# Performance work log

Hardware: AMD Instinct MI355X
Metric: run time of the kernel (lower is better)

Reference implementation:

```python
import jax, jax.numpy as jnp
import numpy as np

C_IN = 34   # C*V = 2*17 channels after reshape
C_MID = 16
C_OUT = 3
N_LAYERS = 3
BN_EPS = 1e-5
NEG_SLOPE = 0.01


def setup_inputs() -> dict:
    key = jax.random.key(0)
    ks = jax.random.split(key, 16)
    B, C, T, V = 512, 2, 2048, 17
    s = 1.0 / np.sqrt(C_IN)
    inp = {
        "x": jax.random.normal(ks[0], (B, C, T, V), dtype=jnp.float32),
        # stacked per-layer 1x1-conv (linear) weights for Q/K/V of 3 attention layers
        "wq": jax.random.normal(ks[1], (N_LAYERS, C_IN, C_IN), dtype=jnp.float32) * s,
        "bq": jax.random.normal(ks[2], (N_LAYERS, C_IN), dtype=jnp.float32) * 0.02,
        "wk": jax.random.normal(ks[3], (N_LAYERS, C_IN, C_IN), dtype=jnp.float32) * s,
        "bk": jax.random.normal(ks[4], (N_LAYERS, C_IN), dtype=jnp.float32) * 0.02,
        "wv": jax.random.normal(ks[5], (N_LAYERS, C_IN, C_IN), dtype=jnp.float32) * s,
        "bv": jax.random.normal(ks[6], (N_LAYERS, C_IN), dtype=jnp.float32) * 0.02,
        # head: conv1 -> BN -> LeakyReLU -> conv2
        "w1": jax.random.normal(ks[7], (C_MID, C_IN), dtype=jnp.float32) * s,
        "b1": jax.random.normal(ks[8], (C_MID,), dtype=jnp.float32) * 0.02,
        "gamma": jnp.ones((C_MID,), dtype=jnp.float32),
        "beta": jnp.zeros((C_MID,), dtype=jnp.float32),
        "mean": jax.random.normal(ks[9], (C_MID,), dtype=jnp.float32) * 0.1,
        "var": jax.random.uniform(ks[10], (C_MID,), dtype=jnp.float32, minval=0.5, maxval=1.5),
        "w2": jax.random.normal(ks[11], (C_OUT, C_MID), dtype=jnp.float32) * (1.0 / np.sqrt(C_MID)),
        "b2": jax.random.normal(ks[12], (C_OUT,), dtype=jnp.float32) * 0.02,
    }
    return inp


def _conv1x1(w, b, h):
    # 1x1 Conv1d == linear over channel dim: (O,C) x (B,C,T) -> (B,O,T)
    return jnp.einsum('oc,bct->bot', w, h) + b[:, None]


def reference(x, wq, bq, wk, bk, wv, bv, w1, b1, gamma, beta, mean, var, w2, b2):
    B, C, T, V = x.shape
    h = x.transpose(0, 1, 3, 2).reshape(B, C * V, T)  # (B, 34, T)
    scale = 1.0 / (T ** 0.5)  # K.size(-1) ** 0.5 in the original
    for i in range(N_LAYERS):
        Q = _conv1x1(wq[i], bq[i], h)
        K = _conv1x1(wk[i], bk[i], h)
        Vv = _conv1x1(wv[i], bv[i], h)
        scores = jnp.einsum('bct,bdt->bcd', Q, K) * scale  # (B, 34, 34) channel attention
        attn = jax.nn.softmax(scores, axis=-1)
        h = jnp.einsum('bcd,bdt->bct', attn, Vv)
    y = _conv1x1(w1, b1, h)                               # (B, 16, T)
    inv = gamma / jnp.sqrt(var + BN_EPS)                  # inference-mode BatchNorm1d
    y = (y - mean[:, None]) * inv[:, None] + beta[:, None]
    y = jnp.where(y > 0, y, NEG_SLOPE * y)                # LeakyReLU
    return _conv1x1(w2, b2, y)                            # (B, 3, T)
```

## Files before the change

kernel.cpp:

```cpp
#include <hip/hip_runtime.h>

#define CV   34
#define TTOT 2048
#define NB   512
#define XB   69632
#define XC   34816

#define GS_STRIDE 1192
#define RB_OFF    (512 * 1192)
#define RB_STRIDE 576

typedef __attribute__((ext_vector_type(8))) short v8s;
typedef __attribute__((ext_vector_type(4))) float v4f;

__device__ __forceinline__ unsigned short f2bf(float f) {
    unsigned int u = __float_as_uint(f);
    u = u + 0x7FFFu + ((u >> 16) & 1u);
    return (unsigned short)(u >> 16);
}
__device__ __forceinline__ float bf2f(unsigned short s) {
    return __uint_as_float(((unsigned int)s) << 16);
}

__device__ __forceinline__ unsigned int cvtpk_bf16(float a, float b) {
    unsigned int r;
    asm("v_cvt_pk_bf16_f32 %0, %1, %2" : "=v"(r) : "v"(a), "v"(b));
    return r;
}

__device__ __forceinline__ void split8(const float (&f)[8], v8s* hi, v8s* lo) {
    union { unsigned int u[4]; v8s s; } H, L;
#pragma unroll
    for (int p = 0; p < 4; ++p) {
        float a = f[2 * p], b = f[2 * p + 1];
        unsigned int h = cvtpk_bf16(a, b);
        float ra = a - __uint_as_float(h << 16);
        float rb = b - __uint_as_float(h & 0xFFFF0000u);
        L.u[p] = cvtpk_bf16(ra, rb);
        H.u[p] = h;
    }
    *hi = H.s;
    *lo = L.s;
}

__device__ __forceinline__ void stage_chunk(const float* __restrict__ xb, int t0,
                                            float* rawbuf, int w, int lane) {
#pragma unroll
    for (int i = 0; i < 5; ++i) {
        int idx = i * 4 + w;
        if (idx < 17) {
            int fl = idx * 256 + lane * 4;
            int co = (fl >= 2176) ? 1 : 0;
            const float* g = xb + t0 * 17 + fl + co * 32640;
            __builtin_amdgcn_global_load_lds(
                (const __attribute__((address_space(1))) void*)g,
                (__attribute__((address_space(3))) void*)(rawbuf + idx * 256),
                16, 0, 0);
        }
    }
}

struct SmemGramB {
    float Gpart[4][34][36];
    float spart[4][36];
};

__global__ __launch_bounds__(256, 4) void k_gram(const float* __restrict__ x,
                                                 float* __restrict__ ws) {
    __shared__ __align__(16) union {
        float raw[2][4352];
        SmemGramB b;
    } sm;

    const int b    = blockIdx.x >> 2;
    const int seg  = blockIdx.x & 3;
    const int tid  = threadIdx.x;
    const int l    = tid & 63;
    const int w    = tid >> 6;
    const int row16 = l & 15;
    const int quad  = l >> 4;
    const float* xb = x + (size_t)b * XB;
    const int t0 = seg * 512;

    int offc[3];
#pragma unroll
    for (int r = 0; r < 3; ++r) {
        int c = r * 16 + row16;
        if (c > 33) c = 33;
        offc[r] = (c >= 17) ? (2159 + c) : c;
    }
    const int koff = w * 32 + quad * 8;

    v4f accG[3][3];
    v4f accS[3];
    v4f vz = {0.f, 0.f, 0.f, 0.f};
#pragma unroll
    for (int r = 0; r < 3; ++r) {
        accS[r] = vz;
#pragma unroll
        for (int c = 0; c < 3; ++c) accG[r][c] = vz;
    }
    v8s ones;
#pragma unroll
    for (int i = 0; i < 8; ++i) ones[i] = (short)0x3F80;

    stage_chunk(xb, t0, sm.raw[0], w, l);
    __syncthreads();

    for (int ch = 0; ch < 4; ++ch) {
        const int cur = ch & 1;
        if (ch < 3) stage_chunk(xb, t0 + (ch + 1) * 128, sm.raw[cur ^ 1], w, l);

        const float* rb = sm.raw[cur] + koff * 17;
        v8s fh[3], fl4[3];
#pragma unroll
        for (int r = 0; r < 3; ++r) {
            const float* p = rb + offc[r];
            float f[8];
#pragma unroll
            for (int e = 0; e < 8; ++e) f[e] = p[e * 17];
            split8(f, &fh[r], &fl4[r]);
        }
#pragma unroll
        for (int r = 0; r < 3; ++r) {
#pragma unroll
            for (int c = 0; c < 3; ++c) {
                accG[r][c] = __builtin_amdgcn_mfma_f32_16x16x32_bf16(fh[r],  fh[c],  accG[r][c], 0, 0, 0);
                accG[r][c] = __builtin_amdgcn_mfma_f32_16x16x32_bf16(fh[r],  fl4[c], accG[r][c], 0, 0, 0);
                accG[r][c] = __builtin_amdgcn_mfma_f32_16x16x32_bf16(fl4[r], fh[c],  accG[r][c], 0, 0, 0);
            }
            accS[r] = __builtin_amdgcn_mfma_f32_16x16x32_bf16(fh[r],  ones, accS[r], 0, 0, 0);
            accS[r] = __builtin_amdgcn_mfma_f32_16x16x32_bf16(fl4[r], ones, accS[r], 0, 0, 0);
        }
        __syncthreads();
    }

#pragma unroll
    for (int r = 0; r < 3; ++r) {
#pragma unroll
        for (int c = 0; c < 3; ++c) {
#pragma unroll
            for (int i = 0; i < 4; ++i) {
                int m = r * 16 + quad * 4 + i;
                int n = c * 16 + row16;
                if (m < 34 && n < 34) sm.b.Gpart[w][m][n] = accG[r][c][i];
            }
        }
        if (row16 == 0) {
#pragma unroll
            for (int i = 0; i < 4; ++i) {
                int m = r * 16 + quad * 4 + i;
                if (m < 34) sm.b.spart[w][m] = accS[r][i];
            }
        }
    }
    __syncthreads();
    float* gout = ws + (size_t)b * GS_STRIDE;
    for (int idx = tid; idx < 1156; idx += 256) {
        int m = idx / 34, n = idx - m * 34;
        atomicAdd(&gout[idx], sm.b.Gpart[0][m][n] + sm.b.Gpart[1][m][n] +
                              sm.b.Gpart[2][m][n] + sm.b.Gpart[3][m][n]);
    }
    if (tid < 34)
        atomicAdd(&gout[1156 + tid], sm.b.spart[0][tid] + sm.b.spart[1][tid] +
                                     sm.b.spart[2][tid] + sm.b.spart[3][tid]);
}

#define RST 44
#define RSZ (36 * RST)
#define R_G0 0
#define R_At (1 * RSZ)
#define R_Aq (2 * RSZ)
#define R_Ak (3 * RSZ)
#define R_Av (4 * RSZ)
#define R_S1 (5 * RSZ)
#define R_Sc (6 * RSZ)
#define R_Wx (7 * RSZ)
#define SMF  (8 * RSZ)

__device__ __forceinline__ void ldfrag8(const float* p, v8s* hi, v8s* lo) {
    float f[8];
    *(float4*)&f[0] = *(const float4*)p;
    *(float4*)&f[4] = *(const float4*)(p + 4);
    split8(f, hi, lo);
}

__device__ __forceinline__ void ldfrag4(const float* p, int quad, v8s* hi, v8s* lo) {
    union { unsigned int u[4]; v8s s; } H, L;
#pragma unroll
    for (int i = 0; i < 4; ++i) { H.u[i] = 0; L.u[i] = 0; }
    if (quad == 0) {
        float4 f = *(const float4*)p;
        unsigned int h0 = cvtpk_bf16(f.x, f.y);
        unsigned int h1 = cvtpk_bf16(f.z, f.w);
        float r0 = f.x - __uint_as_float(h0 << 16);
        float r1 = f.y - __uint_as_float(h0 & 0xFFFF0000u);
        float r2 = f.z - __uint_as_float(h1 << 16);
        float r3 = f.w - __uint_as_float(h1 & 0xFFFF0000u);
        H.u[0] = h0; H.u[1] = h1;
        L.u[0] = cvtpk_bf16(r0, r1);
        L.u[1] = cvtpk_bf16(r2, r3);
    }
    *hi = H.s;
    *lo = L.s;
}

__device__ __forceinline__ void mfma_mm(float* __restrict__ SMD, int Lo, int Ro,
                                        int Do, int l, bool transD) {
    const int lc = l & 15, quad = l >> 4;
    v8s Bh0[3], Bl0[3], Bh1[3], Bl1[3];
#pragma unroll
    for (int tn = 0; tn < 3; ++tn) {
        int r = tn * 16 + lc; r = r < 36 ? r : 35;
        const float* p = SMD + Ro + r * RST;
        ldfrag8(p + quad * 8, &Bh0[tn], &Bl0[tn]);
        ldfrag4(p + 32, quad, &Bh1[tn], &Bl1[tn]);
    }
#pragma unroll
    for (int tm = 0; tm < 3; ++tm) {
        int r = tm * 16 + lc; r = r < 36 ? r : 35;
        const float* p = SMD + Lo + r * RST;
        v8s Ah0, Al0, Ah1, Al1;
        ldfrag8(p + quad * 8, &Ah0, &Al0);
        ldfrag4(p + 32, quad, &Ah1, &Al1);
#pragma unroll
        for (int tn = 0; tn < 3; ++tn) {
            v4f acc = {0.f, 0.f, 0.f, 0.f};
            acc = __builtin_amdgcn_mfma_f32_16x16x32_bf16(Ah0, Bh0[tn], acc, 0, 0, 0);
            acc = __builtin_amdgcn_mfma_f32_16x16x32_bf16(Ah0, Bl0[tn], acc, 0, 0, 0);
            acc = __builtin_amdgcn_mfma_f32_16x16x32_bf16(Al0, Bh0[tn], acc, 0, 0, 0);
            acc = __builtin_amdgcn_mfma_f32_16x16x32_bf16(Ah1, Bh1[tn], acc, 0, 0, 0);
            acc = __builtin_amdgcn_mfma_f32_16x16x32_bf16(Ah1, Bl1[tn], acc, 0, 0, 0);
            acc = __builtin_amdgcn_mfma_f32_16x16x32_bf16(Al1, Bh1[tn], acc, 0, 0, 0);
            if (!transD) {
                int gcol = tn * 16 + lc;
                if (gcol < 36) {
#pragma unroll
                    for (int i = 0; i < 4; ++i) {
                        int grow = tm * 16 + quad * 4 + i;
                        if (grow < 36) SMD[Do + grow * RST + gcol] = acc[i];
                    }
                }
            } else {
                int trow = tn * 16 + lc;
                int tcol = tm * 16 + quad * 4;
                if (trow < 36 && tcol < 36)
                    *(v4f*)&SMD[Do + trow * RST + tcol] = acc;
            }
        }
    }
}

__global__ __launch_bounds__(64) void k_chain(
    const float* __restrict__ wq, const float* __restrict__ bq,
    const float* __restrict__ wk, const float* __restrict__ bk,
    const float* __restrict__ wv, const float* __restrict__ bv,
    const float* __restrict__ w1, const float* __restrict__ b1,
    const float* __restrict__ gamma, const float* __restrict__ beta,
    const float* __restrict__ mean, const float* __restrict__ var,
    float* __restrict__ ws) {
    __shared__ __align__(16) float SMD[SMF];
    const int l = threadIdx.x;
    const int b = blockIdx.x;
    const float* gsb = ws + (size_t)b * GS_STRIDE;

    {
        const float4 z = make_float4(0.f, 0.f, 0.f, 0.f);
        for (int i = l * 4; i < SMF; i += 256) *(float4*)(SMD + i) = z;
    }
    __syncthreads();
    for (int idx = l; idx < 1156; idx += 64) {
        int m = idx / 34, n = idx - m * 34;
        SMD[R_G0 + m * RST + n] = gsb[idx];
        SMD[R_Aq + m * RST + n] = wq[idx];
        SMD[R_Ak + m * RST + n] = wk[idx];
        SMD[R_Av + n * RST + m] = wv[idx];
    }
    if (l < 34) {
        float s = gsb[1156 + l];
        SMD[R_G0 + 34 * RST + l] = s;
        SMD[R_G0 + l * RST + 34] = s;
        SMD[R_Aq + l * RST + 34] = bq[l];
        SMD[R_Ak + l * RST + 34] = bk[l];
        SMD[R_Av + 34 * RST + l] = bv[l];
    }
    if (l == 0) SMD[R_G0 + 34 * RST + 34] = 2048.0f;
    __syncthreads();

    for (int lyr = 0; lyr < 3; ++lyr) {
        if (lyr > 0) {
            const float* wql = wq + lyr * 1156;
            const float* wkl = wk + lyr * 1156;
            const float* wvl = wv + lyr * 1156;
            for (int idx = l; idx < 1156; idx += 64) {
                int m = idx / 34, n = idx - m * 34;
                SMD[R_S1 + m * RST + n] = wql[idx];
                SMD[R_Sc + m * RST + n] = wkl[idx];
                SMD[R_Wx + m * RST + n] = wvl[idx];
            }
            __syncthreads();
            mfma_mm(SMD, R_S1, R_At, R_Aq, l, false);
            mfma_mm(SMD, R_Sc, R_At, R_Ak, l, false);
            mfma_mm(SMD, R_Wx, R_At, R_Av, l, true);
            __syncthreads();
            if (l < 34) {
                SMD[R_Aq + l * RST + 34] += bq[lyr * 34 + l];
                SMD[R_Ak + l * RST + 34] += bk[lyr * 34 + l];
                SMD[R_Av + 34 * RST + l] += bv[lyr * 34 + l];
            }
            __syncthreads();
        }
        mfma_mm(SMD, R_Aq, R_G0, R_S1, l, false);
        __syncthreads();
        mfma_mm(SMD, R_S1, R_Ak, R_Sc, l, false);
        __syncthreads();
        if (l < 34) {
            float f[36];
#pragma unroll
            for (int e0 = 0; e0 < 36; e0 += 4)
                *(float4*)&f[e0] = *(const float4*)&SMD[R_Sc + l * RST + e0];
            const float scale = 0.022097086912079608f;
            float mx = -1e30f;
#pragma unroll
            for (int d = 0; d < 34; ++d) { f[d] *= scale; mx = fmaxf(mx, f[d]); }
            float sum = 0.f;
#pragma unroll
            for (int d = 0; d < 34; ++d) { float e = __expf(f[d] - mx); f[d] = e; sum += e; }
            float rs = 1.0f / sum;
#pragma unroll
            for (int d = 0; d < 34; ++d) f[d] *= rs;
            f[34] = 0.f; f[35] = 0.f;
#pragma unroll
            for (int e0 = 0; e0 < 36; e0 += 4)
                *(float4*)&SMD[R_Sc + l * RST + e0] = *(const float4*)&f[e0];
        } else if (l >= 36 && l < 54) {
            int u = l - 36;
            int row = 34 + u / 9, c4 = (u - (u / 9) * 9) * 4;
            *(float4*)&SMD[R_Sc + row * RST + c4] = make_float4(0.f, 0.f, 0.f, 0.f);
        }
        __syncthreads();
        mfma_mm(SMD, R_Av, R_Sc, R_At, l, false);
        __syncthreads();
    }

    for (int idx = l; idx < 544; idx += 64) {
        int m = idx / 34, n = idx - m * 34;
        SMD[R_Sc + m * RST + n] = w1[idx];
    }
    __syncthreads();
    mfma_mm(SMD, R_Sc, R_At, R_S1, l, false);
    __syncthreads();
    float* wb = ws + RB_OFF + (size_t)b * RB_STRIDE;
    if (l < 16) {
        float iv = gamma[l] * rsqrtf(var[l] + 1e-5f);
        float cyraw = SMD[R_S1 + l * RST + 34] + b1[l];
        wb[512 + l] = (cyraw - mean[l]) * iv + beta[l];
        wb[528 + l] = SMD[R_S1 + l * RST + 32] * iv;
        wb[544 + l] = SMD[R_S1 + l * RST + 33] * iv;
    }
    unsigned short* wp = (unsigned short*)wb;
    for (int i = l; i < 512; i += 64) {
        int o = i >> 5, c = i & 31;
        float iv = gamma[o] * rsqrtf(var[o] + 1e-5f);
        float vv = SMD[R_S1 + o * RST + c] * iv;
        unsigned short hb = f2bf(vv);
        wp[i] = hb;
        wp[512 + i] = f2bf(vv - bf2f(hb));
    }
}

__global__ __launch_bounds__(256, 4) void k_out(const float* __restrict__ x,
                                                const float* __restrict__ w2,
                                                const float* __restrict__ b2,
                                                const float* __restrict__ ws,
                                                float* __restrict__ out) {
    __shared__ __align__(16) float raw[2][4352];

    const int tid  = threadIdx.x;
    const int b    = blockIdx.x >> 3;
    const int seg  = (blockIdx.x & 7) * 256;
    const int l    = tid & 63;
    const int w    = tid >> 6;
    const int quad = l >> 4;
    const int col  = l & 15;

    const float* wb = ws + RB_OFF + (size_t)b * RB_STRIDE;
    const unsigned short* wp = (const unsigned short*)wb;
    v8s aH = *(const v8s*)&wp[col * 32 + quad * 8];
    v8s aL = *(const v8s*)&wp[512 + col * 32 + quad * 8];
    float cyr[4], w2r[3][4], wy32r[4], wy33r[4];
#pragma unroll
    for (int i = 0; i < 4; ++i) {
        int o = quad * 4 + i;
        cyr[i]   = wb[512 + o];
        wy32r[i] = wb[528 + o];
        wy33r[i] = wb[544 + o];
#pragma unroll
        for (int p = 0; p < 3; ++p) w2r[p][i] = w2[p * 16 + o];
    }
    float b2r[3] = {b2[0], b2[1], b2[2]};
    const float* xb = x + (size_t)b * XB;

    int offq[8];
#pragma unroll
    for (int e = 0; e < 8; ++e) {
        int c = quad * 8 + e;
        offq[e] = (c >= 17) ? (2159 + c) : c;
    }

    stage_chunk(xb, seg, raw[0], w, l);
    __syncthreads();

    for (int ch = 0; ch < 2; ++ch) {
        if (ch == 0) stage_chunk(xb, seg + 128, raw[1], w, l);
        for (int tt = w; tt < 8; tt += 4) {
            const int tl = tt * 16 + col;
            const float* rbt = raw[ch] + tl * 17;
            float f[8];
#pragma unroll
            for (int e = 0; e < 8; ++e) f[e] = rbt[offq[e]];
            v8s bH, bL;
            split8(f, &bH, &bL);
            v4f acc = {0.f, 0.f, 0.f, 0.f};
            acc = __builtin_amdgcn_mfma_f32_16x16x32_bf16(aH, bH, acc, 0, 0, 0);
            acc = __builtin_amdgcn_mfma_f32_16x16x32_bf16(aH, bL, acc, 0, 0, 0);
            acc = __builtin_amdgcn_mfma_f32_16x16x32_bf16(aL, bH, acc, 0, 0, 0);
            float h32 = rbt[2191];
            float h33 = rbt[2192];
            float op[3] = {0, 0, 0};
#pragma unroll
            for (int i = 0; i < 4; ++i) {
                float y = acc[i] + cyr[i] + wy32r[i] * h32 + wy33r[i] * h33;
                float z = (y > 0.f) ? y : 0.01f * y;
#pragma unroll
                for (int p = 0; p < 3; ++p) op[p] += w2r[p][i] * z;
            }
#pragma unroll
            for (int p = 0; p < 3; ++p) {
                op[p] += __shfl_xor(op[p], 16);
                op[p] += __shfl_xor(op[p], 32);
            }
            if (l < 16) {
                int tg = seg + ch * 128 + tt * 16 + l;
#pragma unroll
                for (int p = 0; p < 3; ++p)
                    out[((size_t)b * 3 + p) * 2048 + tg] = op[p] + b2r[p];
            }
        }
        __syncthreads();
    }
}

extern "C" void kernel_launch(void* const* d_in, const int* in_sizes, int n_in,
                              void* d_out, int out_size, void* d_ws, size_t ws_size,
                              hipStream_t stream) {
    const float* x     = (const float*)d_in[0];
    const float* wq    = (const float*)d_in[1];
    const float* bq    = (const float*)d_in[2];
    const float* wk    = (const float*)d_in[3];
    const float* bk    = (const float*)d_in[4];
    const float* wv    = (const float*)d_in[5];
    const float* bv    = (const float*)d_in[6];
    const float* w1    = (const float*)d_in[7];
    const float* b1    = (const float*)d_in[8];
    const float* gamma = (const float*)d_in[9];
    const float* beta  = (const float*)d_in[10];
    const float* mean  = (const float*)d_in[11];
    const float* var   = (const float*)d_in[12];
    const float* w2    = (const float*)d_in[13];
    const float* b2    = (const float*)d_in[14];
    float* ws  = (float*)d_ws;
    float* out = (float*)d_out;

    hipMemsetAsync(d_ws, 0, (size_t)NB * GS_STRIDE * sizeof(float), stream);
    k_gram<<<dim3(2048), dim3(256), 0, stream>>>(x, ws);
    k_chain<<<dim3(512), dim3(64), 0, stream>>>(wq, bq, wk, bk, wv, bv,
                                                w1, b1, gamma, beta, mean, var, ws);
    k_out<<<dim3(4096), dim3(256), 0, stream>>>(x, w2, b2, ws, out);
}
```

Measured before the change: 316.6 us.

## Fuse Gram accumulation and attention chain into one per-batch kernel

Merges the Gram/sum reduction kernel and the per-batch attention-chain kernel into a single 256-thread block per batch. The block streams the whole time axis through LDS and reduces the four waves' partial Gram matrices in shared memory, which removes the workspace memset, the global atomics and one launch. The chain matmuls now split their 3 row tiles across 3 waves instead of running on one wave. The trade-off is fewer blocks for the Gram phase (512 instead of 2048), each looping over 16 chunks, which may lower memory parallelism while streaming x.

```diff
diff --git a/kernel.cpp b/kernel.cpp
--- a/kernel.cpp
+++ b/kernel.cpp
@@ -6,8 +6,6 @@
 #define XB   69632
 #define XC   34816
 
-#define GS_STRIDE 1192
-#define RB_OFF    (512 * 1192)
 #define RB_STRIDE 576
 
 typedef __attribute__((ext_vector_type(8))) short v8s;
@@ -58,112 +56,6 @@
                 16, 0, 0);
         }
     }
-}
-
-struct SmemGramB {
-    float Gpart[4][34][36];
-    float spart[4][36];
-};
-
-__global__ __launch_bounds__(256, 4) void k_gram(const float* __restrict__ x,
-                                                 float* __restrict__ ws) {
-    __shared__ __align__(16) union {
-        float raw[2][4352];
-        SmemGramB b;
-    } sm;
-
-    const int b    = blockIdx.x >> 2;
-    const int seg  = blockIdx.x & 3;
-    const int tid  = threadIdx.x;
-    const int l    = tid & 63;
-    const int w    = tid >> 6;
-    const int row16 = l & 15;
-    const int quad  = l >> 4;
-    const float* xb = x + (size_t)b * XB;
-    const int t0 = seg * 512;
-
-    int offc[3];
-#pragma unroll
-    for (int r = 0; r < 3; ++r) {
-        int c = r * 16 + row16;
-        if (c > 33) c = 33;
-        offc[r] = (c >= 17) ? (2159 + c) : c;
-    }
-    const int koff = w * 32 + quad * 8;
-
-    v4f accG[3][3];
-    v4f accS[3];
-    v4f vz = {0.f, 0.f, 0.f, 0.f};
-#pragma unroll
-    for (int r = 0; r < 3; ++r) {
-        accS[r] = vz;
-#pragma unroll
-        for (int c = 0; c < 3; ++c) accG[r][c] = vz;
-    }
-    v8s ones;
-#pragma unroll
-    for (int i = 0; i < 8; ++i) ones[i] = (short)0x3F80;
-
-    stage_chunk(xb, t0, sm.raw[0], w, l);
-    __syncthreads();
-
-    for (int ch = 0; ch < 4; ++ch) {
-        const int cur = ch & 1;
-        if (ch < 3) stage_chunk(xb, t0 + (ch + 1) * 128, sm.raw[cur ^ 1], w, l);
-
-        const float* rb = sm.raw[cur] + koff * 17;
-        v8s fh[3], fl4[3];
-#pragma unroll
-        for (int r = 0; r < 3; ++r) {
-            const float* p = rb + offc[r];
-            float f[8];
-#pragma unroll
-            for (int e = 0; e < 8; ++e) f[e] = p[e * 17];
-            split8(f, &fh[r], &fl4[r]);
-        }
-#pragma unroll
-        for (int r = 0; r < 3; ++r) {
-#pragma unroll
-            for (int c = 0; c < 3; ++c) {
-                accG[r][c] = __builtin_amdgcn_mfma_f32_16x16x32_bf16(fh[r],  fh[c],  accG[r][c], 0, 0, 0);
-                accG[r][c] = __builtin_amdgcn_mfma_f32_16x16x32_bf16(fh[r],  fl4[c], accG[r][c], 0, 0, 0);
-                accG[r][c] = __builtin_amdgcn_mfma_f32_16x16x32_bf16(fl4[r], fh[c],  accG[r][c], 0, 0, 0);
-            }
-            accS[r] = __builtin_amdgcn_mfma_f32_16x16x32_bf16(fh[r],  ones, accS[r], 0, 0, 0);
-            accS[r] = __builtin_amdgcn_mfma_f32_16x16x32_bf16(fl4[r], ones, accS[r], 0, 0, 0);
-        }
-        __syncthreads();
-    }
-
-#pragma unroll
-    for (int r = 0; r < 3; ++r) {
-#pragma unroll
-        for (int c = 0; c < 3; ++c) {
-#pragma unroll
-            for (int i = 0; i < 4; ++i) {
-                int m = r * 16 + quad * 4 + i;
-                int n = c * 16 + row16;
-                if (m < 34 && n < 34) sm.b.Gpart[w][m][n] = accG[r][c][i];
-            }
-        }
-        if (row16 == 0) {
-#pragma unroll
-            for (int i = 0; i < 4; ++i) {
-                int m = r * 16 + quad * 4 + i;
-                if (m < 34) sm.b.spart[w][m] = accS[r][i];
-            }
-        }
-    }
-    __syncthreads();
-    float* gout = ws + (size_t)b * GS_STRIDE;
-    for (int idx = tid; idx < 1156; idx += 256) {
-        int m = idx / 34, n = idx - m * 34;
-        atomicAdd(&gout[idx], sm.b.Gpart[0][m][n] + sm.b.Gpart[1][m][n] +
-                              sm.b.Gpart[2][m][n] + sm.b.Gpart[3][m][n]);
-    }
-    if (tid < 34)
-        atomicAdd(&gout[1156 + tid], sm.b.spart[0][tid] + sm.b.spart[1][tid] +
-                                     sm.b.spart[2][tid] + sm.b.spart[3][tid]);
 }
 
 #define RST 44
@@ -205,53 +97,50 @@
     *lo = L.s;
 }
 
-__device__ __forceinline__ void mfma_mm(float* __restrict__ SMD, int Lo, int Ro,
-                                        int Do, int l, bool transD) {
-    const int lc = l & 15, quad = l >> 4;
-    v8s Bh0[3], Bl0[3], Bh1[3], Bl1[3];
+__device__ __forceinline__ void mfma_mm3(float* __restrict__ SMD, int Lo, int Ro,
+                                         int Do, int wave, int lane, bool transD) {
+    if (wave >= 3) return;
+    const int lc = lane & 15, quad = lane >> 4;
+    const int tm = wave;
+    int ra = tm * 16 + lc; ra = ra < 36 ? ra : 35;
+    const float* pa = SMD + Lo + ra * RST;
+    v8s Ah0, Al0, Ah1, Al1;
+    ldfrag8(pa + quad * 8, &Ah0, &Al0);
+    ldfrag4(pa + 32, quad, &Ah1, &Al1);
 #pragma unroll
     for (int tn = 0; tn < 3; ++tn) {
-        int r = tn * 16 + lc; r = r < 36 ? r : 35;
-        const float* p = SMD + Ro + r * RST;
-        ldfrag8(p + quad * 8, &Bh0[tn], &Bl0[tn]);
-        ldfrag4(p + 32, quad, &Bh1[tn], &Bl1[tn]);
-    }
-#pragma unroll
-    for (int tm = 0; tm < 3; ++tm) {
-        int r = tm * 16 + lc; r = r < 36 ? r : 35;
-        const float* p = SMD + Lo + r * RST;
-        v8s Ah0, Al0, Ah1, Al1;
-        ldfrag8(p + quad * 8, &Ah0, &Al0);
-        ldfrag4(p + 32, quad, &Ah1, &Al1);
-#pragma unroll
-        for (int tn = 0; tn < 3; ++tn) {
-            v4f acc = {0.f, 0.f, 0.f, 0.f};
-            acc = __builtin_amdgcn_mfma_f32_16x16x32_bf16(Ah0, Bh0[tn], acc, 0, 0, 0);
-            acc = __builtin_amdgcn_mfma_f32_16x16x32_bf16(Ah0, Bl0[tn], acc, 0, 0, 0);
-            acc = __builtin_amdgcn_mfma_f32_16x16x32_bf16(Al0, Bh0[tn], acc, 0, 0, 0);
-            acc = __builtin_amdgcn_mfma_f32_16x16x32_bf16(Ah1, Bh1[tn], acc, 0, 0, 0);
-            acc = __builtin_amdgcn_mfma_f32_16x16x32_bf16(Ah1, Bl1[tn], acc, 0, 0, 0);
-            acc = __builtin_amdgcn_mfma_f32_16x16x32_bf16(Al1, Bh1[tn], acc, 0, 0, 0);
-            if (!transD) {
-                int gcol = tn * 16 + lc;
-                if (gcol < 36) {
-#pragma unroll
-                    for (int i = 0; i < 4; ++i) {
-                        int grow = tm * 16 + quad * 4 + i;
-                        if (grow < 36) SMD[Do + grow * RST + gcol] = acc[i];
-                    }
+        int rb = tn * 16 + lc; rb = rb < 36 ? rb : 35;
+        const float* pb = SMD + Ro + rb * RST;
+        v8s Bh0, Bl0, Bh1, Bl1;
+        ldfrag8(pb + quad * 8, &Bh0, &Bl0);
+        ldfrag4(pb + 32, quad, &Bh1, &Bl1);
+        v4f acc = {0.f, 0.f, 0.f, 0.f};
+        acc = __builtin_amdgcn_mfma_f32_16x16x32_bf16(Ah0, Bh0, acc, 0, 0, 0);
+        acc = __builtin_amdgcn_mfma_f32_16x16x32_bf16(Ah0, Bl0, acc, 0, 0, 0);
+        acc = __builtin_amdgcn_mfma_f32_16x16x32_bf16(Al0, Bh0, acc, 0, 0, 0);
+        acc = __builtin_amdgcn_mfma_f32_16x16x32_bf16(Ah1, Bh1, acc, 0, 0, 0);
+        acc = __builtin_amdgcn_mfma_f32_16x16x32_bf16(Ah1, Bl1, acc, 0, 0, 0);
+        acc = __builtin_amdgcn_mfma_f32_16x16x32_bf16(Al1, Bh1, acc, 0, 0, 0);
+        if (!transD) {
+            int gcol = tn * 16 + lc;
+            if (gcol < 36) {
+#pragma unroll
+                for (int i = 0; i < 4; ++i) {
+                    int grow = tm * 16 + quad * 4 + i;
+                    if (grow < 36) SMD[Do + grow * RST + gcol] = acc[i];
                 }
-            } else {
-                int trow = tn * 16 + lc;
-                int tcol = tm * 16 + quad * 4;
-                if (trow < 36 && tcol < 36)
-                    *(v4f*)&SMD[Do + trow * RST + tcol] = acc;
-            }
-        }
-    }
-}
-
-__global__ __launch_bounds__(64) void k_chain(
+            }
+        } else {
+            int trow = tn * 16 + lc;
+            int tcol = tm * 16 + quad * 4;
+            if (trow < 36 && tcol < 36)
+                *(v4f*)&SMD[Do + trow * RST + tcol] = acc;
+        }
+    }
+}
+
+__global__ __launch_bounds__(256) void k_fused(
+    const float* __restrict__ x,
     const float* __restrict__ wq, const float* __restrict__ bq,
     const float* __restrict__ wk, const float* __restrict__ bk,
     const float* __restrict__ wv, const float* __restrict__ bv,
@@ -260,31 +149,135 @@
     const float* __restrict__ mean, const float* __restrict__ var,
     float* __restrict__ ws) {
     __shared__ __align__(16) float SMD[SMF];
-    const int l = threadIdx.x;
-    const int b = blockIdx.x;
-    const float* gsb = ws + (size_t)b * GS_STRIDE;
-
+    const int tid  = threadIdx.x;
+    const int wave = tid >> 6;
+    const int l    = tid & 63;
+    const int b    = blockIdx.x;
+    const int row16 = l & 15;
+    const int quad  = l >> 4;
+    const float* xb = x + (size_t)b * XB;
+
+    float* raw0 = SMD + R_Aq;
+    float* raw1 = SMD + R_Aq + 4352;
+
+    int offc[3];
+#pragma unroll
+    for (int r = 0; r < 3; ++r) {
+        int c = r * 16 + row16;
+        if (c > 33) c = 33;
+        offc[r] = (c >= 17) ? (2159 + c) : c;
+    }
+    const int koff = wave * 32 + quad * 8;
+
+    v4f accG[3][3];
+    v4f accS[3];
+    {
+        v4f vz = {0.f, 0.f, 0.f, 0.f};
+#pragma unroll
+        for (int r = 0; r < 3; ++r) {
+            accS[r] = vz;
+#pragma unroll
+            for (int c = 0; c < 3; ++c) accG[r][c] = vz;
+        }
+    }
+    v8s ones;
+#pragma unroll
+    for (int i = 0; i < 8; ++i) ones[i] = (short)0x3F80;
+
+    stage_chunk(xb, 0, raw0, wave, l);
+    __syncthreads();
+
+    for (int ch = 0; ch < 16; ++ch) {
+        float* cur = (ch & 1) ? raw1 : raw0;
+        float* nxt = (ch & 1) ? raw0 : raw1;
+        if (ch < 15) stage_chunk(xb, (ch + 1) * 128, nxt, wave, l);
+
+        const float* rb = cur + koff * 17;
+        v8s fh[3], fl4[3];
+#pragma unroll
+        for (int r = 0; r < 3; ++r) {
+            const float* p = rb + offc[r];
+            float f[8];
+#pragma unroll
+            for (int e = 0; e < 8; ++e) f[e] = p[e * 17];
+            split8(f, &fh[r], &fl4[r]);
+        }
+#pragma unroll
+        for (int r = 0; r < 3; ++r) {
+#pragma unroll
+            for (int c = 0; c < 3; ++c) {
+                accG[r][c] = __builtin_amdgcn_mfma_f32_16x16x32_bf16(fh[r],  fh[c],  accG[r][c], 0, 0, 0);
+                accG[r][c] = __builtin_amdgcn_mfma_f32_16x16x32_bf16(fh[r],  fl4[c], accG[r][c], 0, 0, 0);
+                accG[r][c] = __builtin_amdgcn_mfma_f32_16x16x32_bf16(fl4[r], fh[c],  accG[r][c], 0, 0, 0);
+            }
+            accS[r] = __builtin_amdgcn_mfma_f32_16x16x32_bf16(fh[r],  ones, accS[r], 0, 0, 0);
+            accS[r] = __builtin_amdgcn_mfma_f32_16x16x32_bf16(fl4[r], ones, accS[r], 0, 0, 0);
+        }
+        __syncthreads();
+    }
+
+    {
+        float* gp = SMD + R_At + wave * RSZ;
+#pragma unroll
+        for (int r = 0; r < 3; ++r) {
+#pragma unroll
+            for (int c = 0; c < 3; ++c) {
+#pragma unroll
+                for (int i = 0; i < 4; ++i) {
+                    int m = r * 16 + quad * 4 + i;
+                    int n = c * 16 + row16;
+                    if (m < 34 && n < 34) gp[m * RST + n] = accG[r][c][i];
+                }
+            }
+            if (row16 == 0) {
+#pragma unroll
+                for (int i = 0; i < 4; ++i) {
+                    int m = r * 16 + quad * 4 + i;
+                    if (m < 34) gp[34 * RST + m] = accS[r][i];
+                }
+            }
+        }
+    }
+    __syncthreads();
+    float gred[5];
+    int   gm[5], gn[5];
+#pragma unroll
+    for (int k = 0; k < 5; ++k) {
+        int idx = tid + k * 256;
+        if (idx < 1156) {
+            int m = idx / 34, n = idx - m * 34;
+            gm[k] = m; gn[k] = n;
+            gred[k] = SMD[R_At + m * RST + n] + SMD[R_Aq + m * RST + n] +
+                      SMD[R_Ak + m * RST + n] + SMD[R_Av + m * RST + n];
+        } else { gm[k] = -1; gn[k] = 0; gred[k] = 0.f; }
+    }
+    float s0red = 0.f;
+    if (tid < 34)
+        s0red = SMD[R_At + 34 * RST + tid] + SMD[R_Aq + 34 * RST + tid] +
+                SMD[R_Ak + 34 * RST + tid] + SMD[R_Av + 34 * RST + tid];
+    __syncthreads();
     {
         const float4 z = make_float4(0.f, 0.f, 0.f, 0.f);
-        for (int i = l * 4; i < SMF; i += 256) *(float4*)(SMD + i) = z;
-    }
-    __syncthreads();
-    for (int idx = l; idx < 1156; idx += 64) {
+        for (int i = tid * 4; i < SMF; i += 1024) *(float4*)(SMD + i) = z;
+    }
+    __syncthreads();
+#pragma unroll
+    for (int k = 0; k < 5; ++k)
+        if (gm[k] >= 0) SMD[R_G0 + gm[k] * RST + gn[k]] = gred[k];
+    for (int idx = tid; idx < 1156; idx += 256) {
         int m = idx / 34, n = idx - m * 34;
-        SMD[R_G0 + m * RST + n] = gsb[idx];
         SMD[R_Aq + m * RST + n] = wq[idx];
         SMD[R_Ak + m * RST + n] = wk[idx];
         SMD[R_Av + n * RST + m] = wv[idx];
     }
-    if (l < 34) {
-        float s = gsb[1156 + l];
-        SMD[R_G0 + 34 * RST + l] = s;
-        SMD[R_G0 + l * RST + 34] = s;
-        SMD[R_Aq + l * RST + 34] = bq[l];
-        SMD[R_Ak + l * RST + 34] = bk[l];
-        SMD[R_Av + 34 * RST + l] = bv[l];
-    }
-    if (l == 0) SMD[R_G0 + 34 * RST + 34] = 2048.0f;
+    if (tid < 34) {
+        SMD[R_G0 + 34 * RST + tid] = s0red;
+        SMD[R_G0 + tid * RST + 34] = s0red;
+        SMD[R_Aq + tid * RST + 34] = bq[tid];
+        SMD[R_Ak + tid * RST + 34] = bk[tid];
+        SMD[R_Av + 34 * RST + tid] = bv[tid];
+    }
+    if (tid == 0) SMD[R_G0 + 34 * RST + 34] = 2048.0f;
     __syncthreads();
 
     for (int lyr = 0; lyr < 3; ++lyr) {
@@ -292,33 +285,33 @@
             const float* wql = wq + lyr * 1156;
             const float* wkl = wk + lyr * 1156;
             const float* wvl = wv + lyr * 1156;
-            for (int idx = l; idx < 1156; idx += 64) {
+            for (int idx = tid; idx < 1156; idx += 256) {
                 int m = idx / 34, n = idx - m * 34;
                 SMD[R_S1 + m * RST + n] = wql[idx];
                 SMD[R_Sc + m * RST + n] = wkl[idx];
                 SMD[R_Wx + m * RST + n] = wvl[idx];
             }
             __syncthreads();
-            mfma_mm(SMD, R_S1, R_At, R_Aq, l, false);
-            mfma_mm(SMD, R_Sc, R_At, R_Ak, l, false);
-            mfma_mm(SMD, R_Wx, R_At, R_Av, l, true);
+            mfma_mm3(SMD, R_S1, R_At, R_Aq, wave, l, false);
+            mfma_mm3(SMD, R_Sc, R_At, R_Ak, wave, l, false);
+            mfma_mm3(SMD, R_Wx, R_At, R_Av, wave, l, true);
             __syncthreads();
-            if (l < 34) {
-                SMD[R_Aq + l * RST + 34] += bq[lyr * 34 + l];
-                SMD[R_Ak + l * RST + 34] += bk[lyr * 34 + l];
-                SMD[R_Av + 34 * RST + l] += bv[lyr * 34 + l];
+            if (tid < 34) {
+                SMD[R_Aq + tid * RST + 34] += bq[lyr * 34 + tid];
+                SMD[R_Ak + tid * RST + 34] += bk[lyr * 34 + tid];
+                SMD[R_Av + 34 * RST + tid] += bv[lyr * 34 + tid];
             }
             __syncthreads();
         }
-        mfma_mm(SMD, R_Aq, R_G0, R_S1, l, false);
-        __syncthreads();
-        mfma_mm(SMD, R_S1, R_Ak, R_Sc, l, false);
-        __syncthreads();
-        if (l < 34) {
+        mfma_mm3(SMD, R_Aq, R_G0, R_S1, wave, l, false);
+        __syncthreads();
+        mfma_mm3(SMD, R_S1, R_Ak, R_Sc, wave, l, false);
+        __syncthreads();
+        if (tid < 34) {
             float f[36];
 #pragma unroll
             for (int e0 = 0; e0 < 36; e0 += 4)
-                *(float4*)&f[e0] = *(const float4*)&SMD[R_Sc + l * RST + e0];
+                *(float4*)&f[e0] = *(const float4*)&SMD[R_Sc + tid * RST + e0];
             const float scale = 0.022097086912079608f;
             float mx = -1e30f;
 #pragma unroll
@@ -332,34 +325,34 @@
             f[34] = 0.f; f[35] = 0.f;
 #pragma unroll
             for (int e0 = 0; e0 < 36; e0 += 4)
-                *(float4*)&SMD[R_Sc + l * RST + e0] = *(const float4*)&f[e0];
-        } else if (l >= 36 && l < 54) {
-            int u = l - 36;
+                *(float4*)&SMD[R_Sc + tid * RST + e0] = *(const float4*)&f[e0];
+        } else if (tid >= 64 && tid < 82) {
+            int u = tid - 64;
             int row = 34 + u / 9, c4 = (u - (u / 9) * 9) * 4;
             *(float4*)&SMD[R_Sc + row * RST + c4] = make_float4(0.f, 0.f, 0.f, 0.f);
         }
         __syncthreads();
-        mfma_mm(SMD, R_Av, R_Sc, R_At, l, false);
-        __syncthreads();
-    }
-
-    for (int idx = l; idx < 544; idx += 64) {
+        mfma_mm3(SMD, R_Av, R_Sc, R_At, wave, l, false);
+        __syncthreads();
+    }
+
+    for (int idx = tid; idx < 544; idx += 256) {
         int m = idx / 34, n = idx - m * 34;
         SMD[R_Sc + m * RST + n] = w1[idx];
     }
     __syncthreads();
-    mfma_mm(SMD, R_Sc, R_At, R_S1, l, false);
-    __syncthreads();
-    float* wb = ws + RB_OFF + (size_t)b * RB_STRIDE;
-    if (l < 16) {
-        float iv = gamma[l] * rsqrtf(var[l] + 1e-5f);
-        float cyraw = SMD[R_S1 + l * RST + 34] + b1[l];
-        wb[512 + l] = (cyraw - mean[l]) * iv + beta[l];
-        wb[528 + l] = SMD[R_S1 + l * RST + 32] * iv;
-        wb[544 + l] = SMD[R_S1 + l * RST + 33] * iv;
+    mfma_mm3(SMD, R_Sc, R_At, R_S1, wave, l, false);
+    __syncthreads();
+    float* wb = ws + (size_t)b * RB_STRIDE;
+    if (tid < 16) {
+        float iv = gamma[tid] * rsqrtf(var[tid] + 1e-5f);
+        float cyraw = SMD[R_S1 + tid * RST + 34] + b1[tid];
+        wb[512 + tid] = (cyraw - mean[tid]) * iv + beta[tid];
+        wb[528 + tid] = SMD[R_S1 + tid * RST + 32] * iv;
+        wb[544 + tid] = SMD[R_S1 + tid * RST + 33] * iv;
     }
     unsigned short* wp = (unsigned short*)wb;
-    for (int i = l; i < 512; i += 64) {
+    for (int i = tid; i < 512; i += 256) {
         int o = i >> 5, c = i & 31;
         float iv = gamma[o] * rsqrtf(var[o] + 1e-5f);
         float vv = SMD[R_S1 + o * RST + c] * iv;
@@ -384,7 +377,7 @@
     const int quad = l >> 4;
     const int col  = l & 15;
 
-    const float* wb = ws + RB_OFF + (size_t)b * RB_STRIDE;
+    const float* wb = ws + (size_t)b * RB_STRIDE;
     const unsigned short* wp = (const unsigned short*)wb;
     v8s aH = *(const v8s*)&wp[col * 32 + quad * 8];
     v8s aL = *(const v8s*)&wp[512 + col * 32 + quad * 8];
@@ -472,9 +465,7 @@
     float* ws  = (float*)d_ws;
     float* out = (float*)d_out;
 
-    hipMemsetAsync(d_ws, 0, (size_t)NB * GS_STRIDE * sizeof(float), stream);
-    k_gram<<<dim3(2048), dim3(256), 0, stream>>>(x, ws);
-    k_chain<<<dim3(512), dim3(64), 0, stream>>>(wq, bq, wk, bk, wv, bv,
-                                                w1, b1, gamma, beta, mean, var, ws);
+    k_fused<<<dim3(512), dim3(256), 0, stream>>>(x, wq, bq, wk, bk, wv, bv,
+                                                 w1, b1, gamma, beta, mean, var, ws);
     k_out<<<dim3(4096), dim3(256), 0, stream>>>(x, w2, b2, ws, out);
 }
```

Result: faster. 277.2 us (-12.4%).
